# Performance work log

Measured on AMD Instinct MI355X. Metric: run time of the kernel, lower is better.

## Reference

```python
import jax, jax.numpy as jnp
import numpy as np

ALPHA = 0.2
BN_EPS = 1e-5
NEG = -9e15


def make_quaternion_mul(kernel):
    # kernel: [in/4, out]; split columns into quaternion components
    dim = kernel.shape[1] // 4
    r, i, j, k = jnp.split(kernel, 4, axis=1)
    r2 = jnp.concatenate([r, -i, -j, -k], axis=0)
    i2 = jnp.concatenate([i, r, -k, j], axis=0)
    j2 = jnp.concatenate([j, k, r, -i], axis=0)
    k2 = jnp.concatenate([k, -j, i, r], axis=0)
    return jnp.concatenate([r2, i2, j2, k2], axis=1)  # [in, out]


def setup_inputs() -> dict:
    key = jax.random.key(0)
    k1, k2, k3, k4 = jax.random.split(key, 4)
    N, IN, OUT = 8192, 512, 128
    inp = jax.random.normal(k1, (N, IN), dtype=jnp.float32)
    adj = jax.random.randint(k2, (N, N), 0, 2, dtype=jnp.int32)
    # xavier-like init for params
    W = jax.random.normal(k3, (IN // 4, OUT), dtype=jnp.float32) * (1.0 / np.sqrt(IN // 4))
    a = jax.random.normal(k4, (2 * OUT, 1), dtype=jnp.float32) * (1.0 / np.sqrt(2 * OUT))
    bn_gamma = jnp.ones((OUT,), dtype=jnp.float32)
    bn_beta = jnp.zeros((OUT,), dtype=jnp.float32)
    return {"input": inp, "adj": adj, "W": W, "a": a, "bn_gamma": bn_gamma, "bn_beta": bn_beta}


def reference(input, adj, W, a, bn_gamma, bn_beta):
    out_features = W.shape[1]
    hamilton = make_quaternion_mul(W)           # [in, out]
    h = input @ hamilton                        # [N, out]
    # a_input[i,j] = concat(h_i, h_j); a_input @ a decomposes as
    # (h @ a1)_i + (h @ a2)_j with a1 = a[:out], a2 = a[out:]
    a1 = a[:out_features, 0]                    # [out]
    a2 = a[out_features:, 0]                    # [out]
    s1 = h @ a1                                 # [N]
    s2 = h @ a2                                 # [N]
    e = s1[:, None] + s2[None, :]               # [N, N]
    e = jnp.where(e > 0, e, ALPHA * e)          # leaky_relu
    attention = jnp.where(adj > 0, e, NEG)
    attention = jax.nn.softmax(attention, axis=1)
    # dropout is identity in inference
    h_prime = attention @ h                     # [N, out]
    # BatchNorm1d (training-mode batch statistics, biased variance)
    mean = jnp.mean(h_prime, axis=0)
    var = jnp.var(h_prime, axis=0)
    h_prime = (h_prime - mean) / jnp.sqrt(var + BN_EPS) * bn_gamma + bn_beta
    # concat=True -> ELU
    return jax.nn.elu(h_prime)
```

## Files before the change

kernel.cpp:

```cpp
#include <hip/hip_runtime.h>
#include <hip/hip_bf16.h>
#include <math.h>

#define N_NODES 8192
#define IN_F    512
#define OUT_F   128
#define LRELU_A 0.2f
#define EPS_BN  1e-5f
#define MSH     40.0f
#define NSPLIT  8
#define JSPAN   (N_NODES / NSPLIT)
#define TILE_I  64
#define ISTR    520

typedef unsigned short u16;
typedef unsigned int   u32;
typedef unsigned long long u64;
typedef __attribute__((ext_vector_type(8))) short  short8;
typedef __attribute__((ext_vector_type(4))) float  floatx4;

__device__ __forceinline__ u16 f2bf_rtn(float x) {
    u32 u = __float_as_uint(x);
    return (u16)((u + 0x7fffu + ((u >> 16) & 1u)) >> 16);
}

#define BALLOT4(vv, rr, MM) do {                                   \
    u64 b0 = __ballot((int)(vv).x > 0);                            \
    u64 b1 = __ballot((int)(vv).y > 0);                            \
    u64 b2 = __ballot((int)(vv).z > 0);                            \
    u64 b3 = __ballot((int)(vv).w > 0);                            \
    if (n == (rr)) {                                               \
        MM[0] = (u32)b0; MM[1] = (u32)(b0 >> 32);                  \
        MM[2] = (u32)b1; MM[3] = (u32)(b1 >> 32);                  \
        MM[4] = (u32)b2; MM[5] = (u32)(b2 >> 32);                  \
        MM[6] = (u32)b3; MM[7] = (u32)(b3 >> 32);                  \
    }                                                              \
} while (0)

__global__ __launch_bounds__(256) void k_hamT(const float* __restrict__ W, u16* __restrict__ hamF,
                                              float* __restrict__ s1, float* __restrict__ s2,
                                              float* __restrict__ cs, float* __restrict__ cq) {
    const int idx = blockIdx.x * 256 + threadIdx.x;
    if (idx < N_NODES) { s1[idx] = 0.f; s2[idx] = 0.f; }
    if (idx < OUT_F)   { cs[idx] = 0.f; cq[idx] = 0.f; }
    const int c = idx >> 9, k = idx & 511;
    const int b = c >> 5, cc = c & 31, kp = k >> 7, kq = k & 127;
    const u32 NEGMASK = 0x284Eu;
    const float sg = ((NEGMASK >> (b * 4 + kp)) & 1u) ? -1.f : 1.f;
    const int kappa = k >> 5, q = (k >> 3) & 3, e = k & 7;
    hamF[((kappa * 4 + q) * 128 + c) * 8 + e] = f2bf_rtn(sg * W[kq * 128 + (b ^ kp) * 32 + cc]);
}

__global__ __launch_bounds__(256) void k_h(const float* __restrict__ inp, const u16* __restrict__ hamF,
                                           const float* __restrict__ a,
                                           u16* __restrict__ hT, float* __restrict__ s1, float* __restrict__ s2) {
    __shared__ u16 inA[16 * ISTR];
    __shared__ float red[4][128][20];
    const int t = threadIdx.x;
    const int lane = t & 63, wid = t >> 6;
    const int quad = lane >> 4, n = lane & 15;
    const int i0 = blockIdx.x * 16;
    const int kb = wid * 128;

#pragma unroll
    for (int u = 0; u < 8; ++u) {
        float4 v = *(const float4*)&inp[(size_t)i0 * IN_F + u * 1024 + t * 4];
        const int r = u * 2 + (t >> 7);
        const int col = (t & 127) * 4;
        u64 pk = (u64)f2bf_rtn(v.x) | ((u64)f2bf_rtn(v.y) << 16)
               | ((u64)f2bf_rtn(v.z) << 32) | ((u64)f2bf_rtn(v.w) << 48);
        *(u64*)&inA[r * ISTR + col] = pk;
    }
    __syncthreads();

    floatx4 acc[8];
#pragma unroll
    for (int ct = 0; ct < 8; ++ct) acc[ct] = (floatx4){0.f, 0.f, 0.f, 0.f};

#pragma unroll
    for (int ks = 0; ks < 4; ++ks) {
        short8 fa = *(const short8*)&inA[n * ISTR + kb + ks * 32 + quad * 8];
#pragma unroll
        for (int ct = 0; ct < 8; ++ct) {
            short8 fb = *(const short8*)&hamF[((wid * 4 + ks) * 4 + quad) * 1024 + (ct * 16 + n) * 8];
            acc[ct] = __builtin_amdgcn_mfma_f32_16x16x32_bf16(fa, fb, acc[ct], 0, 0, 0);
        }
    }

    {
        float p1[4] = {0.f, 0.f, 0.f, 0.f}, p2[4] = {0.f, 0.f, 0.f, 0.f};
#pragma unroll
        for (int ct = 0; ct < 8; ++ct) {
            const int c = ct * 16 + n;
            const float a1v = a[c], a2v = a[OUT_F + c];
#pragma unroll
            for (int r = 0; r < 4; ++r) { p1[r] += acc[ct][r] * a1v; p2[r] += acc[ct][r] * a2v; }
        }
#pragma unroll
        for (int m = 1; m < 16; m <<= 1) {
#pragma unroll
            for (int r = 0; r < 4; ++r) {
                p1[r] += __shfl_xor(p1[r], m, 64);
                p2[r] += __shfl_xor(p2[r], m, 64);
            }
        }
        if (n == 0) {
#pragma unroll
            for (int r = 0; r < 4; ++r) {
                atomicAdd(&s1[i0 + quad * 4 + r], p1[r]);
                atomicAdd(&s2[i0 + quad * 4 + r], p2[r]);
            }
        }
    }

#pragma unroll
    for (int ct = 0; ct < 8; ++ct)
        *(float4*)&red[wid][ct * 16 + n][quad * 4] = *(float4*)&acc[ct];
    __syncthreads();

    {
        const int c = t >> 1, ih = (t & 1) * 8;
        float v[8];
#pragma unroll
        for (int e = 0; e < 8; ++e)
            v[e] = red[0][c][ih + e] + red[1][c][ih + e] + red[2][c][ih + e] + red[3][c][ih + e];
        uint4 pk;
        pk.x = (u32)f2bf_rtn(v[0]) | ((u32)f2bf_rtn(v[1]) << 16);
        pk.y = (u32)f2bf_rtn(v[2]) | ((u32)f2bf_rtn(v[3]) << 16);
        pk.z = (u32)f2bf_rtn(v[4]) | ((u32)f2bf_rtn(v[5]) << 16);
        pk.w = (u32)f2bf_rtn(v[6]) | ((u32)f2bf_rtn(v[7]) << 16);
        *(uint4*)&hT[(size_t)c * N_NODES + i0 + ih] = pk;
    }
}

__global__ __launch_bounds__(256, 4) void k_att(const int* __restrict__ adj, const u16* __restrict__ hT,
                                                const float* __restrict__ s1, const float* __restrict__ s2,
                                                float* __restrict__ Opart, float* __restrict__ Lpart) {
    __shared__ u16 hs[2][128 * 64];
    __shared__ float s2s[JSPAN];
    const int t = threadIdx.x;
    const int lane = t & 63, wid = t >> 6;
    const int quad = lane >> 4, n = lane & 15;
    const int i0 = blockIdx.x * TILE_I;
    const int jbase = blockIdx.y * JSPAN;
    const int i_lane = i0 + wid * 16 + n;
    const float s1v = s1[i_lane];
    const int scr = t >> 3, scj = (t & 7) * 8;

    *(float4*)&s2s[t * 4] = *(const float4*)&s2[jbase + t * 4];

    const size_t rowbase = (size_t)(i0 + wid * 16);
    const int* aj = adj + jbase + lane * 4;

    u32 Mc[8], Mn[8];
#pragma unroll
    for (int w = 0; w < 8; ++w) { Mc[w] = 0u; Mn[w] = 0u; }
#pragma unroll
    for (int b = 0; b < 4; ++b) {
        uint4 vv[4];
#pragma unroll
        for (int r = 0; r < 4; ++r)
            vv[r] = *(const uint4*)(aj + (rowbase + b * 4 + r) * N_NODES);
#pragma unroll
        for (int r = 0; r < 4; ++r) BALLOT4(vv[r], b * 4 + r, Mc);
    }

#pragma unroll
    for (int ps = 0; ps < 4; ++ps) {
        const int cr = ps * 32 + scr;
        uint4 v = *(const uint4*)&hT[(size_t)cr * N_NODES + jbase + scj];
        *(uint4*)&hs[0][cr * 64 + (scj ^ ((cr & 7) * 8))] = v;
    }
    __syncthreads();

    floatx4 acc[8];
#pragma unroll
    for (int ct = 0; ct < 8; ct++) acc[ct] = (floatx4){0.f, 0.f, 0.f, 0.f};
    float Lacc = 0.f;

    uint4 vp[4];

#pragma unroll
    for (int g = 0; g < 4; ++g) {
        if (g > 0) {
#pragma unroll
            for (int r = 0; r < 4; ++r) BALLOT4(vp[r], 12 + r, Mn);
#pragma unroll
            for (int w = 0; w < 8; ++w) Mc[w] = Mn[w];
        }
#pragma unroll
        for (int chi = 0; chi < 4; ++chi) {
            const int ch = g * 4 + chi;
            const int cur = ch & 1;
            const bool more = (ch + 1 < 16);
            if (g < 3) {
                if (chi >= 1) {
#pragma unroll
                    for (int r = 0; r < 4; ++r) BALLOT4(vp[r], (chi - 1) * 4 + r, Mn);
                }
#pragma unroll
                for (int r = 0; r < 4; ++r)
                    vp[r] = *(const uint4*)(aj + (rowbase + chi * 4 + r) * N_NODES + (g + 1) * 256);
            }
            uint4 H[4];
            if (more) {
#pragma unroll
                for (int ps = 0; ps < 4; ++ps) {
                    const int cr = ps * 32 + scr;
                    H[ps] = *(const uint4*)&hT[(size_t)cr * N_NODES + jbase + (ch + 1) * 64 + scj];
                }
            }
            short8 fa[2];
#pragma unroll
            for (int ks = 0; ks < 2; ++ks) {
                const int jl = ch * 64 + ks * 32 + quad * 8;
                float4 sa = *(const float4*)&s2s[jl];
                float4 sb = *(const float4*)&s2s[jl + 4];
                const float sv[8] = {sa.x, sa.y, sa.z, sa.w, sb.x, sb.y, sb.z, sb.w};
                union { u32 u[4]; short8 s; } cv;
#pragma unroll
                for (int jh = 0; jh < 4; ++jh) {
                    float w2[2];
#pragma unroll
                    for (int e = 0; e < 2; ++e) {
                        const int jj = jh * 2 + e;
                        const u32 word = Mc[(jj & 3) * 2 + (chi >> 1)];
                        const int sh = (chi & 1) * 16 + ks * 8 + quad * 2 + (jj >> 2);
                        const u32 mbit = (word >> sh) & 1u;
                        float sc = s1v + sv[jj];
                        sc = fmaxf(sc, LRELU_A * sc);
                        float w = mbit ? __expf(sc - MSH) : 0.f;
                        Lacc += w;
                        w2[e] = w;
                    }
                    cv.u[jh] = (u32)f2bf_rtn(w2[0]) | ((u32)f2bf_rtn(w2[1]) << 16);
                }
                fa[ks] = cv.s;
            }
#pragma unroll
            for (int ct = 0; ct < 8; ++ct) {
                const int rb = ct * 16 + n;
                const int sw = (rb & 7) * 8;
                short8 fb0 = *(const short8*)&hs[cur][rb * 64 + ((quad * 8) ^ sw)];
                short8 fb1 = *(const short8*)&hs[cur][rb * 64 + ((32 + quad * 8) ^ sw)];
                acc[ct] = __builtin_amdgcn_mfma_f32_16x16x32_bf16(fa[0], fb0, acc[ct], 0, 0, 0);
                acc[ct] = __builtin_amdgcn_mfma_f32_16x16x32_bf16(fa[1], fb1, acc[ct], 0, 0, 0);
            }
            if (more) {
#pragma unroll
                for (int ps = 0; ps < 4; ++ps) {
                    const int cr = ps * 32 + scr;
                    *(uint4*)&hs[cur ^ 1][cr * 64 + (scj ^ ((cr & 7) * 8))] = H[ps];
                }
            }
            __syncthreads();
        }
    }

    Lacc += __shfl_xor(Lacc, 16, 64);
    Lacc += __shfl_xor(Lacc, 32, 64);
    if (lane < 16)
        Lpart[(size_t)blockIdx.y * N_NODES + i_lane] = Lacc;

    const size_t obase = (size_t)blockIdx.y * N_NODES * OUT_F;
#pragma unroll
    for (int ct = 0; ct < 8; ++ct) {
#pragma unroll
        for (int r = 0; r < 4; ++r) {
            const int i = i0 + wid * 16 + quad * 4 + r;
            Opart[obase + (size_t)i * OUT_F + ct * 16 + n] = acc[ct][r];
        }
    }
}

__global__ __launch_bounds__(256) void k_comb(const float* __restrict__ Opart, const float* __restrict__ Lpart,
                                              float* __restrict__ hp, float* __restrict__ cs, float* __restrict__ cq) {
    const int t = threadIdx.x;
    const int c = t & 127, half = t >> 7;
    const int ibase = blockIdx.x * 16;
    float sv = 0.f, sq = 0.f;
    for (int k = 0; k < 8; k++) {
        const int i = ibase + half + (k << 1);
        float o = 0.f, L = 0.f;
#pragma unroll
        for (int s = 0; s < NSPLIT; s++) {
            o += Opart[((size_t)s * N_NODES + i) * OUT_F + c];
            L += Lpart[(size_t)s * N_NODES + i];
        }
        float v = L > 0.f ? o / L : 0.f;
        hp[(size_t)i * OUT_F + c] = v;
        sv += v; sq += v * v;
    }
    __shared__ float red[256];
    red[t] = sv; __syncthreads();
    if (half == 0) atomicAdd(&cs[c], sv + red[t + 128]);
    __syncthreads(); red[t] = sq; __syncthreads();
    if (half == 0) atomicAdd(&cq[c], sq + red[t + 128]);
}

__global__ __launch_bounds__(256) void k_bn(const float* __restrict__ hp, const float* __restrict__ cs,
                                            const float* __restrict__ cq, const float* __restrict__ gamma,
                                            const float* __restrict__ beta, float* __restrict__ out) {
    const int idx = blockIdx.x * 256 + threadIdx.x;
    const int c = idx & 127;
    const float mean = cs[c] * (1.f / N_NODES);
    const float var  = cq[c] * (1.f / N_NODES) - mean * mean;
    float x = (hp[idx] - mean) * rsqrtf(var + EPS_BN) * gamma[c] + beta[c];
    x = x > 0.f ? x : expm1f(x);
    out[idx] = x;
}

extern "C" void kernel_launch(void* const* d_in, const int* in_sizes, int n_in,
                              void* d_out, int out_size, void* d_ws, size_t ws_size,
                              hipStream_t stream) {
    (void)in_sizes; (void)n_in; (void)out_size; (void)ws_size;
    const float* inp   = (const float*)d_in[0];
    const int*   adj   = (const int*)d_in[1];
    const float* W     = (const float*)d_in[2];
    const float* a     = (const float*)d_in[3];
    const float* gamma = (const float*)d_in[4];
    const float* beta  = (const float*)d_in[5];
    float* out = (float*)d_out;

    char* wsb = (char*)d_ws;
    u16*   hamF = (u16*)wsb;   wsb += (size_t)OUT_F * IN_F * 2;
    u16*   hT   = (u16*)wsb;   wsb += (size_t)OUT_F * N_NODES * 2;
    float* s1   = (float*)wsb; wsb += N_NODES * 4;
    float* s2   = (float*)wsb; wsb += N_NODES * 4;
    float* Op   = (float*)wsb; wsb += (size_t)NSPLIT * N_NODES * OUT_F * 4;
    float* Lp   = (float*)wsb; wsb += (size_t)NSPLIT * N_NODES * 4;
    float* hp   = (float*)wsb; wsb += (size_t)N_NODES * OUT_F * 4;
    float* cs   = (float*)wsb; wsb += OUT_F * 4;
    float* cq   = (float*)wsb; wsb += OUT_F * 4;

    hipLaunchKernelGGL(k_hamT, dim3(256), dim3(256), 0, stream, W, hamF, s1, s2, cs, cq);
    hipLaunchKernelGGL(k_h,    dim3(512), dim3(256), 0, stream, inp, hamF, a, hT, s1, s2);
    hipLaunchKernelGGL(k_att,  dim3(128, NSPLIT), dim3(256), 0, stream, adj, hT, s1, s2, Op, Lp);
    hipLaunchKernelGGL(k_comb, dim3(512), dim3(256), 0, stream, Op, Lp, hp, cs, cq);
    hipLaunchKernelGGL(k_bn,   dim3(4096), dim3(256), 0, stream, hp, cs, cq, gamma, beta, out);
}
```

Measured before the change: 447.2 us.

## Double j-splits and load full adjacency mask up front instead of pipelined prefetch

Raises the number of j-splits from 8 to 16, so each attention block covers 512 columns (two 256-column groups). Each block now loads and ballots its whole adjacency tile into registers before the compute loop, replacing the software-pipelined per-group prefetch. This doubles the grid's parallelism and removes the interleaved prefetch logic. In exchange, adj load latency is no longer hidden behind MFMA work, and twice as many partial outputs must be written and merged later.

```diff
diff --git a/kernel.cpp b/kernel.cpp
--- a/kernel.cpp
+++ b/kernel.cpp
@@ -8,8 +8,9 @@
 #define LRELU_A 0.2f
 #define EPS_BN  1e-5f
 #define MSH     40.0f
-#define NSPLIT  8
+#define NSPLIT  16
 #define JSPAN   (N_NODES / NSPLIT)
+#define NGRP    (JSPAN / 256)
 #define TILE_I  64
 #define ISTR    520
 
@@ -147,22 +148,26 @@
     const float s1v = s1[i_lane];
     const int scr = t >> 3, scj = (t & 7) * 8;
 
-    *(float4*)&s2s[t * 4] = *(const float4*)&s2[jbase + t * 4];
-
-    const size_t rowbase = (size_t)(i0 + wid * 16);
-    const int* aj = adj + jbase + lane * 4;
-
-    u32 Mc[8], Mn[8];
-#pragma unroll
-    for (int w = 0; w < 8; ++w) { Mc[w] = 0u; Mn[w] = 0u; }
-#pragma unroll
-    for (int b = 0; b < 4; ++b) {
-        uint4 vv[4];
-#pragma unroll
-        for (int r = 0; r < 4; ++r)
-            vv[r] = *(const uint4*)(aj + (rowbase + b * 4 + r) * N_NODES);
-#pragma unroll
-        for (int r = 0; r < 4; ++r) BALLOT4(vv[r], b * 4 + r, Mc);
+    if (t < JSPAN / 4)
+        *(float4*)&s2s[t * 4] = *(const float4*)&s2[jbase + t * 4];
+
+    u32 M[NGRP][8];
+#pragma unroll
+    for (int g = 0; g < NGRP; ++g)
+#pragma unroll
+        for (int w = 0; w < 8; ++w) M[g][w] = 0u;
+    {
+        const size_t rowbase = (size_t)(i0 + wid * 16);
+        const int* aj = adj + jbase + lane * 4;
+#pragma unroll 4
+        for (int rr = 0; rr < 16; ++rr) {
+            const int* ap = aj + (rowbase + rr) * N_NODES;
+            uint4 v[NGRP];
+#pragma unroll
+            for (int g = 0; g < NGRP; ++g) v[g] = *(const uint4*)(ap + g * 256);
+#pragma unroll
+            for (int g = 0; g < NGRP; ++g) BALLOT4(v[g], rr, M[g]);
+        }
     }
 
 #pragma unroll
@@ -178,30 +183,13 @@
     for (int ct = 0; ct < 8; ct++) acc[ct] = (floatx4){0.f, 0.f, 0.f, 0.f};
     float Lacc = 0.f;
 
-    uint4 vp[4];
-
-#pragma unroll
-    for (int g = 0; g < 4; ++g) {
-        if (g > 0) {
-#pragma unroll
-            for (int r = 0; r < 4; ++r) BALLOT4(vp[r], 12 + r, Mn);
-#pragma unroll
-            for (int w = 0; w < 8; ++w) Mc[w] = Mn[w];
-        }
+#pragma unroll
+    for (int g = 0; g < NGRP; ++g) {
 #pragma unroll
         for (int chi = 0; chi < 4; ++chi) {
             const int ch = g * 4 + chi;
             const int cur = ch & 1;
-            const bool more = (ch + 1 < 16);
-            if (g < 3) {
-                if (chi >= 1) {
-#pragma unroll
-                    for (int r = 0; r < 4; ++r) BALLOT4(vp[r], (chi - 1) * 4 + r, Mn);
-                }
-#pragma unroll
-                for (int r = 0; r < 4; ++r)
-                    vp[r] = *(const uint4*)(aj + (rowbase + chi * 4 + r) * N_NODES + (g + 1) * 256);
-            }
+            const bool more = (ch + 1 < NGRP * 4);
             uint4 H[4];
             if (more) {
 #pragma unroll
@@ -224,7 +212,7 @@
 #pragma unroll
                     for (int e = 0; e < 2; ++e) {
                         const int jj = jh * 2 + e;
-                        const u32 word = Mc[(jj & 3) * 2 + (chi >> 1)];
+                        const u32 word = M[g][(jj & 3) * 2 + (chi >> 1)];
                         const int sh = (chi & 1) * 16 + ks * 8 + quad * 2 + (jj >> 2);
                         const u32 mbit = (word >> sh) & 1u;
                         float sc = s1v + sv[jj];
```

Result: no change. 441.8 us (median of 2 runs) (-1.2%).
